# Kernel tuning notes

Hardware: AMD Instinct MI355X
Metric: run time of the kernel (lower is better)

The kernel has to match this reference:

```python
import jax, jax.numpy as jnp
import numpy as np

RCR = 5.2
RCA = 3.5
NUM_SPECIES = 4


def _triu_index(ns):
    i, j = np.triu_indices(ns)
    t = np.zeros((ns, ns), dtype=np.int32)
    idx = np.arange(len(i), dtype=np.int32)
    t[i, j] = idx
    t[j, i] = idx
    return jnp.asarray(t)


TRIU_INDEX = _triu_index(NUM_SPECIES)


def setup_inputs() -> dict:
    key = jax.random.key(0)
    k1, k2 = jax.random.split(key)
    B, N = 128, 32
    coordinates = jax.random.uniform(k1, (B, N, 3), dtype=jnp.float32) * 6.0  # ~6A box
    species = jax.random.randint(k2, (B, N), 0, NUM_SPECIES, dtype=jnp.int32)
    EtaR = jnp.array([16.0], dtype=jnp.float32)
    ShfR = jnp.linspace(0.9, 4.93125, 16, dtype=jnp.float32)
    EtaA = jnp.array([8.0], dtype=jnp.float32)
    Zeta = jnp.array([32.0], dtype=jnp.float32)
    ShfA = jnp.linspace(0.9, 2.85, 4, dtype=jnp.float32)
    ShfZ = jnp.linspace(0.19634954, 2.94524311, 8, dtype=jnp.float32)
    return {"coordinates": coordinates, "EtaR": EtaR, "ShfR": ShfR, "EtaA": EtaA,
            "Zeta": Zeta, "ShfA": ShfA, "ShfZ": ShfZ, "species": species}


def _aev(coordinates, EtaR, ShfR, EtaA, Zeta, ShfA, ShfZ, species):
    B, N, _ = coordinates.shape
    valid = species >= 0
    sp = jnp.clip(species, 0, NUM_SPECIES - 1)
    # pairwise vectors v[b,i,j] = r_j - r_i  (vector from central atom i to j)
    vec = coordinates[:, None, :, :] - coordinates[:, :, None, :]  # (B,N,N,3)
    d2 = jnp.sum(vec * vec, axis=-1)
    eye = jnp.eye(N, dtype=bool)
    d = jnp.sqrt(jnp.where(d2 > 0, d2, 1.0))  # safe sqrt, diag masked below
    pair_ok = valid[:, :, None] & valid[:, None, :] & (~eye)[None]

    # ---- radial AEV: eq (3) ----
    mR = pair_ok & (d <= RCR)
    fcR = 0.5 * jnp.cos(d * (np.pi / RCR)) + 0.5
    # (B,N,N,E,S): 0.25*exp(-EtaR*(d-ShfR)^2)*fc
    rt = 0.25 * jnp.exp(-EtaR[:, None] * (d[..., None, None] - ShfR[None, :]) ** 2) * fcR[..., None, None]
    rt = rt * mR[..., None, None].astype(rt.dtype)
    rt = rt.reshape(B, N, N, -1)  # (B,N,N,16)
    oh = jax.nn.one_hot(species, NUM_SPECIES, dtype=rt.dtype)  # (B,N,4); -1 -> all-zero
    radial = jnp.einsum('bijr,bjs->bisr', rt, oh).reshape(B, N, -1)  # (B,N,64)

    # ---- angular AEV: eq (4), summed over unordered neighbor pairs ----
    mA = pair_ok & (d <= RCA)
    tmask = mA[:, :, :, None] & mA[:, :, None, :] & (~eye)[None, None, :, :]  # (B,N,N,N), j!=k
    dij = d[:, :, :, None]
    dik = d[:, :, None, :]
    cosang = jnp.einsum('bijd,bikd->bijk', vec, vec) / jnp.maximum(dij * dik, 1e-10)
    ang = jnp.arccos(0.95 * cosang)  # (B,N,N,N)
    fcA = 0.5 * jnp.cos(d * (np.pi / RCA)) + 0.5
    fprod = fcA[:, :, :, None] * fcA[:, :, None, :]
    dmean = (dij + dik) * 0.5
    A, Z, P, T = EtaA.shape[0], Zeta.shape[0], ShfA.shape[0], ShfZ.shape[0]
    # factor1: ((1+cos(theta-ShfZ))/2)^Zeta -> (B,N,N,N,Z,T)
    f1 = ((1.0 + jnp.cos(ang[..., None, None] - ShfZ[None, :])) * 0.5) ** Zeta[:, None]
    # factor2: exp(-EtaA*((dij+dik)/2 - ShfA)^2) -> (B,N,N,N,A,P)
    f2 = jnp.exp(-EtaA[:, None] * (dmean[..., None, None] - ShfA[None, :]) ** 2)
    # (B,N,N,N,A,Z,P,T) then flatten sublength in (EtaA,Zeta,ShfA,ShfZ) order
    term = 2.0 * f1[..., None, :, None, :] * f2[..., :, None, :, None] \
        * (fprod * tmask.astype(f1.dtype))[..., None, None, None, None]
    term = term.reshape(B, N, N, N, A * Z * P * T)  # (B,N,N,N,32)
    npairs = NUM_SPECIES * (NUM_SPECIES + 1) // 2
    pidx = TRIU_INDEX[sp[:, :, None], sp[:, None, :]]  # (B,N,N) species-pair bucket
    poh = jax.nn.one_hot(pidx, npairs, dtype=term.dtype)  # (B,N,N,10)
    # 0.5: ordered (j,k) double-counts the symmetric unordered pairs
    angular = 0.5 * jnp.einsum('bijkf,bjkp->bipf', term, poh)
    angular = angular.reshape(B, N, -1)  # (B,N,320)

    return jnp.concatenate([radial, angular], axis=-1)  # (B,N,384)


def reference(coordinates, EtaR, ShfR, EtaA, Zeta, ShfA, ShfZ, species):
    return _aev(coordinates, EtaR, ShfR, EtaA, Zeta, ShfA, ShfZ, species)
```

## Files before the change

kernel.cpp:

```cpp
#include <hip/hip_runtime.h>
#include <math.h>

#define NATOM   32
#define NSP     4
#define NPAIRS  (NATOM * (NATOM - 1) / 2)
#define NCLS    10
#define NSHFR   16
#define NSHFA   4
#define NSHFZ   8
#define FEAT_ANG (NSHFA * NSHFZ)
#define OUT_PER_ATOM (NSP * NSHFR + NCLS * FEAT_ANG)

#define RCR_F 5.2f
#define RCA_F 3.5f
#define PI_F  3.14159265358979323846f

template <bool FAST>
__device__ __forceinline__ void angular_accum(
    const float2* __restrict__ pc_cs, const float* __restrict__ pc_ef,
    int s0, int e0, int p, float ct, float st, float zt, float& acc)
{
    for (int pp = s0; pp < e0; ++pp) {
        const float2 cs = pc_cs[pp];
        const float  ee = pc_ef[pp * 4 + p];
        const float u = fmaf(cs.x, ct, fmaf(cs.y, st, 0.5f));
        float f1;
        if (FAST) {
            const float u2 = u * u, u4 = u2 * u2, u8 = u4 * u4, u16 = u8 * u8;
            f1 = u16 * u16;
        } else {
            f1 = __powf(fmaxf(u, 0.f), zt);
        }
        acc = fmaf(f1, ee, acc);
    }
}

__device__ __constant__ int STRIPE_CLS[4][3] = {
    {0, 1, 4}, {2, 3, -1}, {5, 6, -1}, {7, 8, 9}
};

__global__ __launch_bounds__(128) void aev_kernel(
    const float* __restrict__ coords,
    const float* __restrict__ etaR,
    const float* __restrict__ shfR,
    const float* __restrict__ etaA,
    const float* __restrict__ zeta,
    const float* __restrict__ shfA,
    const float* __restrict__ shfZ,
    const int*   __restrict__ species,
    float* __restrict__ out)
{
    const int atom = blockIdx.x;
    const int b    = atom >> 5;
    const int i    = atom & 31;
    const int tid  = threadIdx.x;

    __shared__ float svx[NATOM], svy[NATOM], svz[NATOM];
    __shared__ float sd[NATOM], sfcA[NATOM], sfcR[NATOM];
    __shared__ int   ssp[NATOM];
    __shared__ float2 pc_cs[NPAIRS];
    __shared__ float4 pc_e[NPAIRS];
    __shared__ int   s_cnt[NCLS];
    __shared__ int   s_wp[NCLS];

    const float cix = coords[(b * NATOM + i) * 3 + 0];
    const float ciy = coords[(b * NATOM + i) * 3 + 1];
    const float ciz = coords[(b * NATOM + i) * 3 + 2];
    const int   spi = species[b * NATOM + i];

    if (tid < NATOM) {
        const int j = tid;
        const float x = coords[(b * NATOM + j) * 3 + 0];
        const float y = coords[(b * NATOM + j) * 3 + 1];
        const float z = coords[(b * NATOM + j) * 3 + 2];
        const float vx = x - cix, vy = y - ciy, vz = z - ciz;
        const float d2 = vx * vx + vy * vy + vz * vz;
        const float d  = sqrtf(d2 > 0.f ? d2 : 1.f);
        const int spj = species[b * NATOM + j];
        const bool ok = (j != i) && (spj >= 0) && (spi >= 0);
        const float fcA = (ok && d <= RCA_F) ? (0.5f * __cosf(d * (PI_F / RCA_F)) + 0.5f) : 0.f;
        const float fcR = (ok && d <= RCR_F) ? (0.5f * __cosf(d * (PI_F / RCR_F)) + 0.5f) : 0.f;
        svx[j] = vx; svy[j] = vy; svz[j] = vz;
        sd[j] = d; sfcA[j] = fcA; sfcR[j] = fcR;
        ssp[j] = spj < 0 ? 0 : (spj > (NSP - 1) ? (NSP - 1) : spj);
    }
    if (tid < NCLS) s_cnt[tid] = 0;
    __syncthreads();

    const long obase = (long)atom * OUT_PER_ATOM;

    if (tid < 64) {
        const int r  = tid & 15;
        const int jg = tid >> 4;
        const float shf = shfR[r];
        const float eta = etaR[0];
        float a0 = 0.f, a1 = 0.f, a2 = 0.f, a3 = 0.f;
        for (int j = jg; j < NATOM; j += 4) {
            const float fc = sfcR[j];
            if (fc > 0.f) {
                const float dd = sd[j] - shf;
                const float v = 0.25f * __expf(-eta * dd * dd) * fc;
                const int s = ssp[j];
                a0 += (s == 0) ? v : 0.f;
                a1 += (s == 1) ? v : 0.f;
                a2 += (s == 2) ? v : 0.f;
                a3 += (s == 3) ? v : 0.f;
            }
        }
        a0 += __shfl_xor(a0, 16); a0 += __shfl_xor(a0, 32);
        a1 += __shfl_xor(a1, 16); a1 += __shfl_xor(a1, 32);
        a2 += __shfl_xor(a2, 16); a2 += __shfl_xor(a2, 32);
        a3 += __shfl_xor(a3, 16); a3 += __shfl_xor(a3, 32);
        if (tid < 16) {
            out[obase + 0 * NSHFR + r] = a0;
            out[obase + 1 * NSHFR + r] = a1;
            out[obase + 2 * NSHFR + r] = a2;
            out[obase + 3 * NSHFR + r] = a3;
        }
    }

    int   cache_w[4];
    float cache_fac[4];

#pragma unroll
    for (int cc = 0; cc < 4; ++cc) {
        const int pid = cc * 128 + tid;
        bool act = false; int j = 0, k = 0, cls = 0; float fac = 0.f;
        if (pid < NPAIRS) {
            j = (int)((63.0f - sqrtf((float)(3969 - 8 * pid))) * 0.5f);
            int Sj = j * 31 - ((j * (j - 1)) >> 1);
            if (Sj > pid) { --j; Sj = j * 31 - ((j * (j - 1)) >> 1); }
            else {
                const int Sn = (j + 1) * 31 - (((j + 1) * j) >> 1);
                if (Sn <= pid) { j += 1; Sj = Sn; }
            }
            k = j + 1 + (pid - Sj);
            fac = 2.f * sfcA[j] * sfcA[k];
            if (fac > 0.f) {
                act = true;
                const int sj = ssp[j], sk = ssp[k];
                const int lo = min(sj, sk), hi = max(sj, sk);
                cls = lo * NSP - ((lo * (lo - 1)) >> 1) + (hi - lo);
                atomicAdd(&s_cnt[cls], 1);
            }
        }
        cache_w[cc] = j | (k << 8) | (cls << 16) | (act ? (1 << 24) : 0);
        cache_fac[cc] = fac;
    }
    __syncthreads();

    int off[NCLS], cntv[NCLS];
    {
        int run = 0;
#pragma unroll
        for (int q = 0; q < NCLS; ++q) { cntv[q] = s_cnt[q]; off[q] = run; run += cntv[q]; }
    }
    if (tid < NCLS) s_wp[tid] = off[tid];
    __syncthreads();

    const float eA  = etaA[0];
    const float sa0 = shfA[0], sa1 = shfA[1], sa2 = shfA[2], sa3 = shfA[3];
#pragma unroll
    for (int cc = 0; cc < 4; ++cc) {
        const int w = cache_w[cc];
        if ((w >> 24) != 0) {
            const int j = w & 0xff, k = (w >> 8) & 0xff, cls = (w >> 16) & 0xff;
            const float fac = cache_fac[cc];
            const float dj = sd[j], dk = sd[k];
            const float dot = svx[j] * svx[k] + svy[j] * svy[k] + svz[j] * svz[k];
            const float c = 0.95f * dot * __builtin_amdgcn_rcpf(fmaxf(dj * dk, 1e-10f));
            const float s = __builtin_amdgcn_sqrtf(fmaxf(1.f - c * c, 0.f));
            const float dm = 0.5f * (dj + dk);
            const float d0 = dm - sa0, d1 = dm - sa1, d2 = dm - sa2, d3 = dm - sa3;
            const float e0 = fac * __expf(-eA * d0 * d0);
            const float e1 = fac * __expf(-eA * d1 * d1);
            const float e2 = fac * __expf(-eA * d2 * d2);
            const float e3 = fac * __expf(-eA * d3 * d3);
            const int pos = atomicAdd(&s_wp[cls], 1);
            pc_cs[pos] = make_float2(0.5f * c, 0.5f * s);
            pc_e[pos]  = make_float4(e0, e1, e2, e3);
        }
    }
    __syncthreads();

    {
        const int f = tid & 31;
        const int p = f >> 3;
        const int t = f & 7;
        const int stripe = tid >> 5;
        float st, ct;
        __sincosf(shfZ[t], &st, &ct);
        const float zt = zeta[0];
        const float* pc_ef = (const float*)pc_e;
        float* oang = out + obase + NSP * NSHFR;

        if (zt == 32.0f) {
#pragma unroll
            for (int s = 0; s < 3; ++s) {
                const int q = STRIPE_CLS[stripe][s];
                if (q >= 0) {
                    float acc = 0.f;
                    angular_accum<true>(pc_cs, pc_ef, off[q], off[q] + cntv[q], p, ct, st, zt, acc);
                    oang[q * FEAT_ANG + f] = acc;
                }
            }
        } else {
#pragma unroll
            for (int s = 0; s < 3; ++s) {
                const int q = STRIPE_CLS[stripe][s];
                if (q >= 0) {
                    float acc = 0.f;
                    angular_accum<false>(pc_cs, pc_ef, off[q], off[q] + cntv[q], p, ct, st, zt, acc);
                    oang[q * FEAT_ANG + f] = acc;
                }
            }
        }
    }
}

extern "C" void kernel_launch(void* const* d_in, const int* in_sizes, int n_in,
                              void* d_out, int out_size, void* d_ws, size_t ws_size,
                              hipStream_t stream) {
    const float* coords  = (const float*)d_in[0];
    const float* etaR    = (const float*)d_in[1];
    const float* shfR    = (const float*)d_in[2];
    const float* etaA    = (const float*)d_in[3];
    const float* zeta    = (const float*)d_in[4];
    const float* shfA    = (const float*)d_in[5];
    const float* shfZ    = (const float*)d_in[6];
    const int*   species = (const int*)d_in[7];
    float* out = (float*)d_out;

    const int B = in_sizes[0] / (NATOM * 3);
    aev_kernel<<<B * NATOM, 128, 0, stream>>>(coords, etaR, shfR, etaA, zeta,
                                              shfA, shfZ, species, out);
}
```

Baseline: 89.54 us.

## Process two central atoms per block and store angular radial terms in half precision

Each 256-thread block now handles two central atoms instead of one atom per 128-thread block, so shared-memory tables, pair enumeration and class bucketing are duplicated per atom within one block. The four radial-shift exponential factors of each angular pair are stored as fp16 in shared memory to cut LDS footprint and bandwidth. Class offsets move from per-thread registers to shared memory. The aim is to amortize block launch and setup and to raise occupancy, at the cost of reduced precision in the angular exponential factors and more shared-memory reads in the inner loop.

```diff
diff --git a/kernel.cpp b/kernel.cpp
--- a/kernel.cpp
+++ b/kernel.cpp
@@ -1,4 +1,5 @@
 #include <hip/hip_runtime.h>
+#include <hip/hip_fp16.h>
 #include <math.h>
 
 #define NATOM   32
@@ -10,6 +11,7 @@
 #define NSHFZ   8
 #define FEAT_ANG (NSHFA * NSHFZ)
 #define OUT_PER_ATOM (NSP * NSHFR + NCLS * FEAT_ANG)
+#define NAB     2
 
 #define RCR_F 5.2f
 #define RCA_F 3.5f
@@ -17,12 +19,12 @@
 
 template <bool FAST>
 __device__ __forceinline__ void angular_accum(
-    const float2* __restrict__ pc_cs, const float* __restrict__ pc_ef,
+    const float2* __restrict__ pc_cs, const __half* __restrict__ pc_eh,
     int s0, int e0, int p, float ct, float st, float zt, float& acc)
 {
     for (int pp = s0; pp < e0; ++pp) {
         const float2 cs = pc_cs[pp];
-        const float  ee = pc_ef[pp * 4 + p];
+        const float  ee = __half2float(pc_eh[pp * 4 + p]);
         const float u = fmaf(cs.x, ct, fmaf(cs.y, st, 0.5f));
         float f1;
         if (FAST) {
@@ -39,7 +41,7 @@
     {0, 1, 4}, {2, 3, -1}, {5, 6, -1}, {7, 8, 9}
 };
 
-__global__ __launch_bounds__(128) void aev_kernel(
+__global__ __launch_bounds__(256, 8) void aev_kernel(
     const float* __restrict__ coords,
     const float* __restrict__ etaR,
     const float* __restrict__ shfR,
@@ -50,157 +52,175 @@
     const int*   __restrict__ species,
     float* __restrict__ out)
 {
-    const int atom = blockIdx.x;
-    const int b    = atom >> 5;
-    const int i    = atom & 31;
-    const int tid  = threadIdx.x;
-
-    __shared__ float svx[NATOM], svy[NATOM], svz[NATOM];
-    __shared__ float sd[NATOM], sfcA[NATOM], sfcR[NATOM];
+    const int a0  = blockIdx.x * NAB;
+    const int b   = a0 >> 5;
+    const int i0  = a0 & 31;
+    const int tid = threadIdx.x;
+
+    __shared__ float svx[NAB * NATOM], svy[NAB * NATOM], svz[NAB * NATOM];
+    __shared__ float sd[NAB * NATOM], sfcA[NAB * NATOM], sfcR[NAB * NATOM];
     __shared__ int   ssp[NATOM];
-    __shared__ float2 pc_cs[NPAIRS];
-    __shared__ float4 pc_e[NPAIRS];
-    __shared__ int   s_cnt[NCLS];
-    __shared__ int   s_wp[NCLS];
-
-    const float cix = coords[(b * NATOM + i) * 3 + 0];
-    const float ciy = coords[(b * NATOM + i) * 3 + 1];
-    const float ciz = coords[(b * NATOM + i) * 3 + 2];
-    const int   spi = species[b * NATOM + i];
-
-    if (tid < NATOM) {
-        const int j = tid;
+    __shared__ float2 pc_cs[NAB * NPAIRS];
+    __shared__ __align__(8) __half pc_eh[NAB * NPAIRS * 4];
+    __shared__ int   s_cnt[NAB * NCLS];
+    __shared__ int   s_off[NAB * NCLS];
+    __shared__ int   s_wpr[NAB * NCLS];
+
+    if (tid < NAB * NATOM) {
+        const int c = tid >> 5;
+        const int j = tid & 31;
+        const int ic = i0 + c;
+        const float cx = coords[(b * NATOM + ic) * 3 + 0];
+        const float cy = coords[(b * NATOM + ic) * 3 + 1];
+        const float cz = coords[(b * NATOM + ic) * 3 + 2];
+        const int spi = species[b * NATOM + ic];
         const float x = coords[(b * NATOM + j) * 3 + 0];
         const float y = coords[(b * NATOM + j) * 3 + 1];
         const float z = coords[(b * NATOM + j) * 3 + 2];
-        const float vx = x - cix, vy = y - ciy, vz = z - ciz;
+        const float vx = x - cx, vy = y - cy, vz = z - cz;
         const float d2 = vx * vx + vy * vy + vz * vz;
         const float d  = sqrtf(d2 > 0.f ? d2 : 1.f);
         const int spj = species[b * NATOM + j];
-        const bool ok = (j != i) && (spj >= 0) && (spi >= 0);
+        const bool ok = (j != ic) && (spj >= 0) && (spi >= 0);
         const float fcA = (ok && d <= RCA_F) ? (0.5f * __cosf(d * (PI_F / RCA_F)) + 0.5f) : 0.f;
         const float fcR = (ok && d <= RCR_F) ? (0.5f * __cosf(d * (PI_F / RCR_F)) + 0.5f) : 0.f;
-        svx[j] = vx; svy[j] = vy; svz[j] = vz;
-        sd[j] = d; sfcA[j] = fcA; sfcR[j] = fcR;
-        ssp[j] = spj < 0 ? 0 : (spj > (NSP - 1) ? (NSP - 1) : spj);
-    }
-    if (tid < NCLS) s_cnt[tid] = 0;
-    __syncthreads();
-
-    const long obase = (long)atom * OUT_PER_ATOM;
-
-    if (tid < 64) {
-        const int r  = tid & 15;
-        const int jg = tid >> 4;
+        const int cj = c * NATOM + j;
+        svx[cj] = vx; svy[cj] = vy; svz[cj] = vz;
+        sd[cj] = d; sfcA[cj] = fcA; sfcR[cj] = fcR;
+        if (c == 0) ssp[j] = spj < 0 ? 0 : (spj > (NSP - 1) ? (NSP - 1) : spj);
+    }
+    if (tid < NAB * NCLS) s_cnt[tid] = 0;
+    __syncthreads();
+
+    if (tid < NAB * 64) {
+        const int c    = tid >> 6;
+        const int lane = tid & 63;
+        const int r  = lane & 15;
+        const int jg = lane >> 4;
         const float shf = shfR[r];
         const float eta = etaR[0];
-        float a0 = 0.f, a1 = 0.f, a2 = 0.f, a3 = 0.f;
+        float a0f = 0.f, a1f = 0.f, a2f = 0.f, a3f = 0.f;
         for (int j = jg; j < NATOM; j += 4) {
-            const float fc = sfcR[j];
+            const float fc = sfcR[c * NATOM + j];
             if (fc > 0.f) {
-                const float dd = sd[j] - shf;
+                const float dd = sd[c * NATOM + j] - shf;
                 const float v = 0.25f * __expf(-eta * dd * dd) * fc;
                 const int s = ssp[j];
-                a0 += (s == 0) ? v : 0.f;
-                a1 += (s == 1) ? v : 0.f;
-                a2 += (s == 2) ? v : 0.f;
-                a3 += (s == 3) ? v : 0.f;
-            }
-        }
-        a0 += __shfl_xor(a0, 16); a0 += __shfl_xor(a0, 32);
-        a1 += __shfl_xor(a1, 16); a1 += __shfl_xor(a1, 32);
-        a2 += __shfl_xor(a2, 16); a2 += __shfl_xor(a2, 32);
-        a3 += __shfl_xor(a3, 16); a3 += __shfl_xor(a3, 32);
-        if (tid < 16) {
-            out[obase + 0 * NSHFR + r] = a0;
-            out[obase + 1 * NSHFR + r] = a1;
-            out[obase + 2 * NSHFR + r] = a2;
-            out[obase + 3 * NSHFR + r] = a3;
-        }
-    }
-
-    int   cache_w[4];
-    float cache_fac[4];
+                a0f += (s == 0) ? v : 0.f;
+                a1f += (s == 1) ? v : 0.f;
+                a2f += (s == 2) ? v : 0.f;
+                a3f += (s == 3) ? v : 0.f;
+            }
+        }
+        a0f += __shfl_xor(a0f, 16); a0f += __shfl_xor(a0f, 32);
+        a1f += __shfl_xor(a1f, 16); a1f += __shfl_xor(a1f, 32);
+        a2f += __shfl_xor(a2f, 16); a2f += __shfl_xor(a2f, 32);
+        a3f += __shfl_xor(a3f, 16); a3f += __shfl_xor(a3f, 32);
+        if (lane < 16) {
+            const long ob = (long)(a0 + c) * OUT_PER_ATOM;
+            out[ob + 0 * NSHFR + r] = a0f;
+            out[ob + 1 * NSHFR + r] = a1f;
+            out[ob + 2 * NSHFR + r] = a2f;
+            out[ob + 3 * NSHFR + r] = a3f;
+        }
+    }
+
+    int   wv[4];
+    float facs[4];
 
 #pragma unroll
     for (int cc = 0; cc < 4; ++cc) {
-        const int pid = cc * 128 + tid;
-        bool act = false; int j = 0, k = 0, cls = 0; float fac = 0.f;
-        if (pid < NPAIRS) {
-            j = (int)((63.0f - sqrtf((float)(3969 - 8 * pid))) * 0.5f);
+        const int slot = cc * 256 + tid;
+        bool act = false; int j = 0, k = 0, cls = 0, c = 0; float fac = 0.f;
+        if (slot < NAB * NPAIRS) {
+            c = (slot >= NPAIRS) ? 1 : 0;
+            const int lp = slot - c * NPAIRS;
+            j = (int)((63.0f - sqrtf((float)(3969 - 8 * lp))) * 0.5f);
             int Sj = j * 31 - ((j * (j - 1)) >> 1);
-            if (Sj > pid) { --j; Sj = j * 31 - ((j * (j - 1)) >> 1); }
+            if (Sj > lp) { --j; Sj = j * 31 - ((j * (j - 1)) >> 1); }
             else {
                 const int Sn = (j + 1) * 31 - (((j + 1) * j) >> 1);
-                if (Sn <= pid) { j += 1; Sj = Sn; }
-            }
-            k = j + 1 + (pid - Sj);
-            fac = 2.f * sfcA[j] * sfcA[k];
+                if (Sn <= lp) { j += 1; Sj = Sn; }
+            }
+            k = j + 1 + (lp - Sj);
+            fac = 2.f * sfcA[c * NATOM + j] * sfcA[c * NATOM + k];
             if (fac > 0.f) {
                 act = true;
                 const int sj = ssp[j], sk = ssp[k];
                 const int lo = min(sj, sk), hi = max(sj, sk);
                 cls = lo * NSP - ((lo * (lo - 1)) >> 1) + (hi - lo);
-                atomicAdd(&s_cnt[cls], 1);
-            }
-        }
-        cache_w[cc] = j | (k << 8) | (cls << 16) | (act ? (1 << 24) : 0);
-        cache_fac[cc] = fac;
-    }
-    __syncthreads();
-
-    int off[NCLS], cntv[NCLS];
-    {
+                atomicAdd(&s_cnt[c * NCLS + cls], 1);
+            }
+        }
+        wv[cc]   = j | (k << 8) | (cls << 16) | (act ? (1 << 24) : 0) | (c << 25);
+        facs[cc] = fac;
+    }
+    __syncthreads();
+
+    if (tid < NAB) {
         int run = 0;
-#pragma unroll
-        for (int q = 0; q < NCLS; ++q) { cntv[q] = s_cnt[q]; off[q] = run; run += cntv[q]; }
-    }
-    if (tid < NCLS) s_wp[tid] = off[tid];
+        const int base = tid * NCLS;
+#pragma unroll
+        for (int q = 0; q < NCLS; ++q) {
+            s_off[base + q] = run;
+            s_wpr[base + q] = run;
+            run += s_cnt[base + q];
+        }
+    }
     __syncthreads();
 
     const float eA  = etaA[0];
     const float sa0 = shfA[0], sa1 = shfA[1], sa2 = shfA[2], sa3 = shfA[3];
 #pragma unroll
     for (int cc = 0; cc < 4; ++cc) {
-        const int w = cache_w[cc];
-        if ((w >> 24) != 0) {
+        const int w = wv[cc];
+        if ((w >> 24) & 1) {
             const int j = w & 0xff, k = (w >> 8) & 0xff, cls = (w >> 16) & 0xff;
-            const float fac = cache_fac[cc];
-            const float dj = sd[j], dk = sd[k];
-            const float dot = svx[j] * svx[k] + svy[j] * svy[k] + svz[j] * svz[k];
-            const float c = 0.95f * dot * __builtin_amdgcn_rcpf(fmaxf(dj * dk, 1e-10f));
-            const float s = __builtin_amdgcn_sqrtf(fmaxf(1.f - c * c, 0.f));
+            const int c = (w >> 25) & 1;
+            const float fac = facs[cc];
+            const int cj = c * NATOM + j, ck = c * NATOM + k;
+            const float dj = sd[cj], dk = sd[ck];
+            const float dot = svx[cj] * svx[ck] + svy[cj] * svy[ck] + svz[cj] * svz[ck];
+            const float cv = 0.95f * dot * __builtin_amdgcn_rcpf(fmaxf(dj * dk, 1e-10f));
+            const float sv = __builtin_amdgcn_sqrtf(fmaxf(1.f - cv * cv, 0.f));
             const float dm = 0.5f * (dj + dk);
             const float d0 = dm - sa0, d1 = dm - sa1, d2 = dm - sa2, d3 = dm - sa3;
             const float e0 = fac * __expf(-eA * d0 * d0);
             const float e1 = fac * __expf(-eA * d1 * d1);
             const float e2 = fac * __expf(-eA * d2 * d2);
             const float e3 = fac * __expf(-eA * d3 * d3);
-            const int pos = atomicAdd(&s_wp[cls], 1);
-            pc_cs[pos] = make_float2(0.5f * c, 0.5f * s);
-            pc_e[pos]  = make_float4(e0, e1, e2, e3);
+            const int pos = c * NPAIRS + atomicAdd(&s_wpr[c * NCLS + cls], 1);
+            pc_cs[pos] = make_float2(0.5f * cv, 0.5f * sv);
+            __half2* dst = reinterpret_cast<__half2*>(pc_eh + pos * 4);
+            dst[0] = __floats2half2_rn(e0, e1);
+            dst[1] = __floats2half2_rn(e2, e3);
         }
     }
     __syncthreads();
 
     {
-        const int f = tid & 31;
+        const int wave = tid >> 6;
+        const int lane = tid & 63;
+        const int c    = wave >> 1;
+        const int stripe = ((wave & 1) << 1) | (lane >> 5);
+        const int f = lane & 31;
         const int p = f >> 3;
         const int t = f & 7;
-        const int stripe = tid >> 5;
         float st, ct;
         __sincosf(shfZ[t], &st, &ct);
         const float zt = zeta[0];
-        const float* pc_ef = (const float*)pc_e;
-        float* oang = out + obase + NSP * NSHFR;
+        float* oang = out + (long)(a0 + c) * OUT_PER_ATOM + NSP * NSHFR;
+        const int cbase = c * NPAIRS;
 
         if (zt == 32.0f) {
 #pragma unroll
             for (int s = 0; s < 3; ++s) {
                 const int q = STRIPE_CLS[stripe][s];
                 if (q >= 0) {
+                    const int o = cbase + s_off[c * NCLS + q];
+                    const int n = s_cnt[c * NCLS + q];
                     float acc = 0.f;
-                    angular_accum<true>(pc_cs, pc_ef, off[q], off[q] + cntv[q], p, ct, st, zt, acc);
+                    angular_accum<true>(pc_cs, pc_eh, o, o + n, p, ct, st, zt, acc);
                     oang[q * FEAT_ANG + f] = acc;
                 }
             }
@@ -209,8 +229,10 @@
             for (int s = 0; s < 3; ++s) {
                 const int q = STRIPE_CLS[stripe][s];
                 if (q >= 0) {
+                    const int o = cbase + s_off[c * NCLS + q];
+                    const int n = s_cnt[c * NCLS + q];
                     float acc = 0.f;
-                    angular_accum<false>(pc_cs, pc_ef, off[q], off[q] + cntv[q], p, ct, st, zt, acc);
+                    angular_accum<false>(pc_cs, pc_eh, o, o + n, p, ct, st, zt, acc);
                     oang[q * FEAT_ANG + f] = acc;
                 }
             }
@@ -232,6 +254,6 @@
     float* out = (float*)d_out;
 
     const int B = in_sizes[0] / (NATOM * 3);
-    aev_kernel<<<B * NATOM, 128, 0, stream>>>(coords, etaR, shfR, etaA, zeta,
-                                              shfA, shfZ, species, out);
+    aev_kernel<<<(B * NATOM) / NAB, 256, 0, stream>>>(coords, etaR, shfR, etaA, zeta,
+                                                      shfA, shfZ, species, out);
 }
```

After: 87.60 us. -2.2%, faster.
